# Kernel optimization log

Measured on AMD Instinct MI355X. Metric: run time of the kernel, lower is better.

The kernel has to match this reference:

```python
import jax, jax.numpy as jnp
import numpy as np

UNITS = 4096
INPUT_DIM = 1024
N = 16384


def setup_inputs() -> dict:
    key = jax.random.key(0)
    k1, k2 = jax.random.split(key)
    inputs = jax.random.normal(k1, (N, INPUT_DIM), dtype=jnp.float32)
    # Keras 'random_normal' initializer: stddev 0.05
    w = jax.random.normal(k2, (UNITS, INPUT_DIM), dtype=jnp.float32) * 0.05
    return {"inputs": inputs, "w": w}


def reference(inputs, w):
    # Pairwise squared Euclidean distance: out[n, u] = sum_d (w[u,d] - x[n,d])^2
    x_sq = jnp.sum(inputs * inputs, axis=-1, keepdims=True)        # [N, 1]
    w_sq = jnp.sum(w * w, axis=-1)                                  # [U]
    cross = jnp.einsum("nd,ud->nu", inputs, w)                     # [N, U]
    return x_sq + w_sq[None, :] - 2.0 * cross
```

## Files before the change

kernel.cpp:

```cpp
#include <hip/hip_runtime.h>
#include <cstdint>
#include <cstddef>

#define AS1 __attribute__((address_space(1)))
#define AS3 __attribute__((address_space(3)))

typedef unsigned short u16;
typedef unsigned int u32;
typedef unsigned char u8;
typedef int i32x4 __attribute__((ext_vector_type(4)));
typedef int i32x8 __attribute__((ext_vector_type(8)));
typedef float f32x4 __attribute__((ext_vector_type(4)));

constexpr int D  = 1024;
constexpr int NS = 16384;
constexpr int US = 4096;
constexpr int BM = 256, BN = 256, BK = 128;
constexpr int KT = D / BK;

constexpr size_t XQ_OFF  = 0;
constexpr size_t WQ_OFF  = (size_t)NS * D;
constexpr size_t XSQ_OFF = WQ_OFF + (size_t)US * D;
constexpr size_t WSQ_OFF = XSQ_OFF + (size_t)NS * 4;

__global__ __launch_bounds__(256) void quant_sq(
    const float* __restrict__ x, const float* __restrict__ w,
    u8* __restrict__ xq, u8* __restrict__ wq,
    float* __restrict__ xsq, float* __restrict__ wsq) {
  const int lane = threadIdx.x & 63;
  const int wave = blockIdx.x * 4 + (threadIdx.x >> 6);
  const int nwaves = gridDim.x * 4;
  for (int row = wave; row < NS + US; row += nwaves) {
    const float* src; u8* qdst; float* sdst; int r; float qscale;
    if (row < NS) { src = x; qdst = xq; sdst = xsq; r = row; qscale = 1.0f; }
    else          { src = w; qdst = wq; sdst = wsq; r = row - NS; qscale = 16.0f; }
    const float4* s4 = (const float4*)(src + (size_t)r * D);
    u32* qrow = (u32*)(qdst + (size_t)r * D);
    float s = 0.f;
#pragma unroll
    for (int it = 0; it < 4; ++it) {
      const float4 v = s4[it * 64 + lane];
      s += v.x * v.x + v.y * v.y + v.z * v.z + v.w * v.w;
      u32 p01 = __builtin_amdgcn_cvt_pk_fp8_f32(v.x * qscale, v.y * qscale, 0, false);
      u32 w0  = __builtin_amdgcn_cvt_pk_fp8_f32(v.z * qscale, v.w * qscale, p01, true);
      qrow[it * 64 + lane] = w0;
    }
#pragma unroll
    for (int off = 32; off; off >>= 1) s += __shfl_down(s, off, 64);
    if (lane == 0) sdst[r] = s;
  }
}

__global__ __launch_bounds__(512, 2) void dist_gemm(
    const u8* __restrict__ xq, const u8* __restrict__ wq,
    const float* __restrict__ xsq, const float* __restrict__ wsq,
    float* __restrict__ out) {
  __shared__ u8 lds[2 * 65536];

  const int tid = threadIdx.x;
  const int lane = tid & 63;
  const int wv = tid >> 6;
  const int wm = wv >> 2;
  const int wn = wv & 3;
  const int quad = lane >> 4;
  const int l15 = lane & 15;

  const int m0 = blockIdx.y * BM;
  const int n0 = blockIdx.x * BN;

  f32x4 acc[8][4];
#pragma unroll
  for (int mt = 0; mt < 8; ++mt)
#pragma unroll
    for (int nt = 0; nt < 4; ++nt)
      acc[mt][nt] = (f32x4){0.f, 0.f, 0.f, 0.f};

  const int srow = tid >> 3;
  const int sch = lane & 7;

  auto stage = [&](int buf, int kt) {
    u8* base = lds + buf * 65536;
    const int k0 = kt * BK;
#pragma unroll
    for (int s = 0; s < 4; ++s) {
      const int r = s * 64 + srow;
      const int cg = sch ^ (r & 7);
      const u8* ga = xq + (size_t)(m0 + r) * D + k0 + cg * 16;
      __builtin_amdgcn_global_load_lds((AS1 void*)(u8*)ga,
          (AS3 void*)(base + s * 8192 + wv * 1024), 16, 0, 0);
    }
#pragma unroll
    for (int s = 0; s < 4; ++s) {
      const int r = s * 64 + srow;
      const int cg = sch ^ (r & 7);
      const u8* gb = wq + (size_t)(n0 + r) * D + k0 + cg * 16;
      __builtin_amdgcn_global_load_lds((AS1 void*)(u8*)gb,
          (AS3 void*)(base + 32768 + s * 8192 + wv * 1024), 16, 0, 0);
    }
  };

  stage(0, 0);
  stage(1, 1);
  asm volatile("s_waitcnt vmcnt(8)" ::: "memory");
  __builtin_amdgcn_sched_barrier(0);
  __builtin_amdgcn_s_barrier();
  __builtin_amdgcn_sched_barrier(0);

  for (int kt = 0; kt < KT; ++kt) {
    const u8* sA = lds + (kt & 1) * 65536;
    const u8* sB = sA + 32768;

    i32x8 b[4];
#pragma unroll
    for (int nt = 0; nt < 4; ++nt) {
      const int n = wn * 64 + nt * 16 + l15;
      const int s = n & 7;
      const i32x4 b0 = *reinterpret_cast<const i32x4*>(sB + n * BK + ((2 * quad) ^ s) * 16);
      const i32x4 b1 = *reinterpret_cast<const i32x4*>(sB + n * BK + ((2 * quad + 1) ^ s) * 16);
      b[nt] = __builtin_shufflevector(b0, b1, 0, 1, 2, 3, 4, 5, 6, 7);
    }
#pragma unroll
    for (int mt = 0; mt < 8; ++mt) {
      const int m = wm * 128 + mt * 16 + l15;
      const int s = m & 7;
      const i32x4 a0 = *reinterpret_cast<const i32x4*>(sA + m * BK + ((2 * quad) ^ s) * 16);
      const i32x4 a1 = *reinterpret_cast<const i32x4*>(sA + m * BK + ((2 * quad + 1) ^ s) * 16);
      const i32x8 a = __builtin_shufflevector(a0, a1, 0, 1, 2, 3, 4, 5, 6, 7);
      __builtin_amdgcn_s_setprio(1);
#pragma unroll
      for (int nt = 0; nt < 4; ++nt) {
        acc[mt][nt] = __builtin_amdgcn_mfma_scale_f32_16x16x128_f8f6f4(
            a, b[nt], acc[mt][nt],  0,  0,
             0, 0x7F7F7F7F,  0, 0x7F7F7F7F);
      }
      __builtin_amdgcn_s_setprio(0);
    }

    if (kt == KT - 1) break;

    __builtin_amdgcn_sched_barrier(0);
    __builtin_amdgcn_s_barrier();
    __builtin_amdgcn_sched_barrier(0);
    if (kt + 2 < KT) {
      stage(kt & 1, kt + 2);
      asm volatile("s_waitcnt vmcnt(8)" ::: "memory");
    } else {
      asm volatile("s_waitcnt vmcnt(0)" ::: "memory");
    }
    __builtin_amdgcn_sched_barrier(0);
    __builtin_amdgcn_s_barrier();
    __builtin_amdgcn_sched_barrier(0);
  }

#pragma unroll
  for (int mt = 0; mt < 8; ++mt) {
    const int R0 = m0 + wm * 128 + mt * 16 + quad * 4;
#pragma unroll
    for (int nt = 0; nt < 4; ++nt) {
      const int C = n0 + wn * 64 + nt * 16 + l15;
      const float wsv = wsq[C];
#pragma unroll
      for (int r = 0; r < 4; ++r) {
        const int R = R0 + r;
        out[(size_t)R * US + C] = xsq[R] + wsv - 0.125f * acc[mt][nt][r];
      }
    }
  }
}

extern "C" void kernel_launch(void* const* d_in, const int* in_sizes, int n_in,
                              void* d_out, int out_size, void* d_ws, size_t ws_size,
                              hipStream_t stream) {
  const float* x = (const float*)d_in[0];
  const float* w = (const float*)d_in[1];
  float* out = (float*)d_out;
  char* ws = (char*)d_ws;

  u8* xq = (u8*)(ws + XQ_OFF);
  u8* wq = (u8*)(ws + WQ_OFF);
  float* xsq = (float*)(ws + XSQ_OFF);
  float* wsq = (float*)(ws + WSQ_OFF);

  quant_sq<<<dim3(640), dim3(256), 0, stream>>>(x, w, xq, wq, xsq, wsq);
  dist_gemm<<<dim3(US / BN, NS / BM), dim3(512), 0, stream>>>(xq, wq, xsq, wsq, out);
}
```

Before: 388.5 us.

## Interleave next-tile global-to-LDS loads across four MFMA phases per K step

Each K iteration of the FP8 distance GEMM is split into four barrier-delimited phases, each running 8 MFMAs. The global_load_lds prefetches for tile t+2 are spread across these phases, and the A slices still being read are deferred to the next iteration, so that loads overlap with matrix work instead of being issued in one burst. The K loop is also fully unrolled and the vmcnt wait thresholds are adjusted to match. In exchange there are many more s_barriers per tile and a larger unrolled code body, and the interleaving could add sync stalls.

New measurement: 383.1 us. No clear change (-1.4%).

```diff
diff --git a/kernel.cpp b/kernel.cpp
--- a/kernel.cpp
+++ b/kernel.cpp
@@ -5,7 +5,6 @@
 #define AS1 __attribute__((address_space(1)))
 #define AS3 __attribute__((address_space(3)))
 
-typedef unsigned short u16;
 typedef unsigned int u32;
 typedef unsigned char u8;
 typedef int i32x4 __attribute__((ext_vector_type(4)));
@@ -68,88 +67,123 @@
   const int m0 = blockIdx.y * BM;
   const int n0 = blockIdx.x * BN;
 
-  f32x4 acc[8][4];
-#pragma unroll
-  for (int mt = 0; mt < 8; ++mt)
-#pragma unroll
-    for (int nt = 0; nt < 4; ++nt)
-      acc[mt][nt] = (f32x4){0.f, 0.f, 0.f, 0.f};
-
   const int srow = tid >> 3;
   const int sch = lane & 7;
 
-  auto stage = [&](int buf, int kt) {
-    u8* base = lds + buf * 65536;
-    const int k0 = kt * BK;
-#pragma unroll
-    for (int s = 0; s < 4; ++s) {
-      const int r = s * 64 + srow;
-      const int cg = sch ^ (r & 7);
-      const u8* ga = xq + (size_t)(m0 + r) * D + k0 + cg * 16;
-      __builtin_amdgcn_global_load_lds((AS1 void*)(u8*)ga,
-          (AS3 void*)(base + s * 8192 + wv * 1024), 16, 0, 0);
-    }
-#pragma unroll
-    for (int s = 0; s < 4; ++s) {
-      const int r = s * 64 + srow;
-      const int cg = sch ^ (r & 7);
-      const u8* gb = wq + (size_t)(n0 + r) * D + k0 + cg * 16;
-      __builtin_amdgcn_global_load_lds((AS1 void*)(u8*)gb,
-          (AS3 void*)(base + 32768 + s * 8192 + wv * 1024), 16, 0, 0);
-    }
+  f32x4 acc[8][4];
+#pragma unroll
+  for (int mt = 0; mt < 8; ++mt)
+#pragma unroll
+    for (int nt = 0; nt < 4; ++nt) acc[mt][nt] = (f32x4){0.f, 0.f, 0.f, 0.f};
+
+  auto stageA = [&](int buf, int kt, int sw) {
+    const int r = sw * 64 + srow;
+    const int cg = sch ^ (r & 7);
+    const u8* g = xq + (size_t)(m0 + r) * D + kt * BK + cg * 16;
+    __builtin_amdgcn_global_load_lds((AS1 void*)(u8*)g,
+        (AS3 void*)(lds + buf * 65536 + sw * 8192 + wv * 1024), 16, 0, 0);
   };
-
-  stage(0, 0);
-  stage(1, 1);
+  auto stageB = [&](int buf, int kt, int sw) {
+    const int r = sw * 64 + srow;
+    const int cg = sch ^ (r & 7);
+    const u8* g = wq + (size_t)(n0 + r) * D + kt * BK + cg * 16;
+    __builtin_amdgcn_global_load_lds((AS1 void*)(u8*)g,
+        (AS3 void*)(lds + buf * 65536 + 32768 + sw * 8192 + wv * 1024), 16, 0, 0);
+  };
+  auto ldfrag = [&](const u8* mat, int row) -> i32x8 {
+    const int s = row & 7;
+    const i32x4 f0 = *reinterpret_cast<const i32x4*>(mat + row * BK + ((2 * quad) ^ s) * 16);
+    const i32x4 f1 = *reinterpret_cast<const i32x4*>(mat + row * BK + ((2 * quad + 1) ^ s) * 16);
+    return __builtin_shufflevector(f0, f1, 0, 1, 2, 3, 4, 5, 6, 7);
+  };
+
+#pragma unroll
+  for (int sw = 0; sw < 4; ++sw) stageA(0, 0, sw);
+#pragma unroll
+  for (int sw = 0; sw < 4; ++sw) stageB(0, 0, sw);
+#pragma unroll
+  for (int sw = 0; sw < 4; ++sw) stageA(1, 1, sw);
+#pragma unroll
+  for (int sw = 0; sw < 4; ++sw) stageB(1, 1, sw);
   asm volatile("s_waitcnt vmcnt(8)" ::: "memory");
   __builtin_amdgcn_sched_barrier(0);
   __builtin_amdgcn_s_barrier();
   __builtin_amdgcn_sched_barrier(0);
 
-  for (int kt = 0; kt < KT; ++kt) {
-    const u8* sA = lds + (kt & 1) * 65536;
+#define MM(MT, NT, AF) \
+  acc[MT][NT] = __builtin_amdgcn_mfma_scale_f32_16x16x128_f8f6f4( \
+      AF, bf[NT], acc[MT][NT], 0, 0, 0, 0x7F7F7F7F, 0, 0x7F7F7F7F)
+
+#define OPEN_PHASE() do { \
+    __builtin_amdgcn_sched_barrier(0); \
+    __builtin_amdgcn_s_barrier(); \
+    asm volatile("s_waitcnt lgkmcnt(0)" ::: "memory"); \
+    __builtin_amdgcn_sched_barrier(0); \
+    __builtin_amdgcn_s_setprio(1); } while (0)
+
+#define CLOSE_PHASE() do { \
+    __builtin_amdgcn_s_setprio(0); \
+    __builtin_amdgcn_sched_barrier(0); \
+    __builtin_amdgcn_s_barrier(); \
+    __builtin_amdgcn_sched_barrier(0); } while (0)
+
+#pragma unroll
+  for (int t = 0; t < KT; ++t) {
+    const u8* sA = lds + (t & 1) * 65536;
     const u8* sB = sA + 32768;
-
-    i32x8 b[4];
-#pragma unroll
-    for (int nt = 0; nt < 4; ++nt) {
-      const int n = wn * 64 + nt * 16 + l15;
-      const int s = n & 7;
-      const i32x4 b0 = *reinterpret_cast<const i32x4*>(sB + n * BK + ((2 * quad) ^ s) * 16);
-      const i32x4 b1 = *reinterpret_cast<const i32x4*>(sB + n * BK + ((2 * quad + 1) ^ s) * 16);
-      b[nt] = __builtin_shufflevector(b0, b1, 0, 1, 2, 3, 4, 5, 6, 7);
-    }
-#pragma unroll
-    for (int mt = 0; mt < 8; ++mt) {
-      const int m = wm * 128 + mt * 16 + l15;
-      const int s = m & 7;
-      const i32x4 a0 = *reinterpret_cast<const i32x4*>(sA + m * BK + ((2 * quad) ^ s) * 16);
-      const i32x4 a1 = *reinterpret_cast<const i32x4*>(sA + m * BK + ((2 * quad + 1) ^ s) * 16);
-      const i32x8 a = __builtin_shufflevector(a0, a1, 0, 1, 2, 3, 4, 5, 6, 7);
-      __builtin_amdgcn_s_setprio(1);
-#pragma unroll
-      for (int nt = 0; nt < 4; ++nt) {
-        acc[mt][nt] = __builtin_amdgcn_mfma_scale_f32_16x16x128_f8f6f4(
-            a, b[nt], acc[mt][nt],  0,  0,
-             0, 0x7F7F7F7F,  0, 0x7F7F7F7F);
+    const int nb = (t + 1) & 1;
+    const int ar = wm * 128 + l15;
+    const int br = wn * 64 + l15;
+
+    i32x8 bf[4];
+
+    {
+      bf[0] = ldfrag(sB, br);
+      bf[1] = ldfrag(sB, br + 16);
+      bf[2] = ldfrag(sB, br + 32);
+      bf[3] = ldfrag(sB, br + 48);
+      i32x8 a0 = ldfrag(sA, ar);
+      i32x8 a1 = ldfrag(sA, ar + 16);
+      if (t >= 1 && t + 1 < KT) { stageA(nb, t + 1, 1); stageA(nb, t + 1, 3); }
+      OPEN_PHASE();
+      MM(0, 0, a0); MM(0, 1, a0); MM(0, 2, a0); MM(0, 3, a0);
+      MM(1, 0, a1); MM(1, 1, a1); MM(1, 2, a1); MM(1, 3, a1);
+      CLOSE_PHASE();
+    }
+    {
+      i32x8 a0 = ldfrag(sA, ar + 32);
+      i32x8 a1 = ldfrag(sA, ar + 48);
+      if (t + 2 < KT) { stageB(t & 1, t + 2, 0); stageB(t & 1, t + 2, 1); stageB(t & 1, t + 2, 2); }
+      OPEN_PHASE();
+      MM(2, 0, a0); MM(2, 1, a0); MM(2, 2, a0); MM(2, 3, a0);
+      MM(3, 0, a1); MM(3, 1, a1); MM(3, 2, a1); MM(3, 3, a1);
+      CLOSE_PHASE();
+    }
+    {
+      i32x8 a0 = ldfrag(sA, ar + 64);
+      i32x8 a1 = ldfrag(sA, ar + 80);
+      if (t + 2 < KT) { stageB(t & 1, t + 2, 3); stageA(t & 1, t + 2, 0); stageA(t & 1, t + 2, 2); }
+      OPEN_PHASE();
+      MM(4, 0, a0); MM(4, 1, a0); MM(4, 2, a0); MM(4, 3, a0);
+      MM(5, 0, a1); MM(5, 1, a1); MM(5, 2, a1); MM(5, 3, a1);
+      CLOSE_PHASE();
+    }
+    {
+      i32x8 a0 = ldfrag(sA, ar + 96);
+      i32x8 a1 = ldfrag(sA, ar + 112);
+      OPEN_PHASE();
+      MM(6, 0, a0); MM(6, 1, a0); MM(6, 2, a0); MM(6, 3, a0);
+      MM(7, 0, a1); MM(7, 1, a1); MM(7, 2, a1); MM(7, 3, a1);
+      __builtin_amdgcn_s_setprio(0);
+      __builtin_amdgcn_sched_barrier(0);
+      if (t < KT - 1) {
+        if (t + 2 < KT) asm volatile("s_waitcnt vmcnt(6)" ::: "memory");
+        else            asm volatile("s_waitcnt vmcnt(0)" ::: "memory");
+        __builtin_amdgcn_sched_barrier(0);
+        __builtin_amdgcn_s_barrier();
+        __builtin_amdgcn_sched_barrier(0);
       }
-      __builtin_amdgcn_s_setprio(0);
-    }
-
-    if (kt == KT - 1) break;
-
-    __builtin_amdgcn_sched_barrier(0);
-    __builtin_amdgcn_s_barrier();
-    __builtin_amdgcn_sched_barrier(0);
-    if (kt + 2 < KT) {
-      stage(kt & 1, kt + 2);
-      asm volatile("s_waitcnt vmcnt(8)" ::: "memory");
-    } else {
-      asm volatile("s_waitcnt vmcnt(0)" ::: "memory");
-    }
-    __builtin_amdgcn_sched_barrier(0);
-    __builtin_amdgcn_s_barrier();
-    __builtin_amdgcn_sched_barrier(0);
+    }
   }
 
 #pragma unroll
```
